# Kernel optimization log

Hardware: AMD Instinct MI355X
Metric: run time of the kernel (lower is better)

## Reference

```python
import jax, jax.numpy as jnp
import numpy as np
import math

EPS = 1e-12


def _cmul(ar, ai, br, bi):
    return ar * br - ai * bi, ar * bi + ai * br


def _wilson_seed(x):
    # x: (B, 4, L, L) -> conj of canonical Wilson-line path, (B, L, L) re/im
    ux_r, ux_i, uy_r, uy_i = x[:, 0], x[:, 1], x[:, 2], x[:, 3]
    B, L, _ = ux_r.shape
    dt = x.dtype

    def step(c, u):
        cr, ci = c
        ur, ui = u
        nr, ni = _cmul(cr, ci, ur, ui)
        return (nr, ni), (nr, ni)

    # cumulative complex product along x at y=0
    init_r = jnp.ones((B,), dt)
    init_i = jnp.zeros((B,), dt)
    xs = (ux_r[:, :-1, 0].T, ux_i[:, :-1, 0].T)  # (L-1, B)
    _, (axr, axi) = jax.lax.scan(step, (init_r, init_i), xs)
    x_axis_r = jnp.concatenate([init_r[None], axr], 0).T  # (B, L)
    x_axis_i = jnp.concatenate([init_i[None], axi], 0).T

    # cumulative complex product along y, vectorized over x
    ys = (jnp.moveaxis(uy_r[:, :, :-1], 2, 0), jnp.moveaxis(uy_i[:, :, :-1], 2, 0))  # (L-1, B, L)
    _, (pr, pi_) = jax.lax.scan(step, (x_axis_r, x_axis_i), ys)
    path_r = jnp.moveaxis(jnp.concatenate([x_axis_r[None], pr], 0), 0, 2)  # (B, L, L)
    path_i = jnp.moveaxis(jnp.concatenate([x_axis_i[None], pi_], 0), 0, 2)
    return path_r, -path_i  # conjugate


def _wrap(t):
    return (t + math.pi) % (2.0 * math.pi) - math.pi


def _initial_features(x):
    seed_r, seed_i = _wilson_seed(x)
    ax = jnp.arctan2(x[:, 1], x[:, 0])
    ay = jnp.arctan2(x[:, 3], x[:, 2])
    plaq = _wrap(ax + jnp.roll(ay, -1, axis=1) - jnp.roll(ax, -1, axis=2) - ay)
    pc = jnp.cos(plaq)
    pavg = (pc + jnp.roll(pc, 1, 1) + jnp.roll(pc, -1, 1)
            + jnp.roll(pc, 1, 2) + jnp.roll(pc, -1, 2)) / 5.0
    scalars = jnp.stack([jnp.ones_like(pc), pc, pavg], axis=1)  # (B, 3, L, L)
    return seed_r[:, None] * scalars, seed_i[:, None] * scalars


def _transport_fwd(fr, fi, x, mu):
    lr, li = (x[:, 0], x[:, 1]) if mu == 0 else (x[:, 2], x[:, 3])
    sr = jnp.roll(fr, -1, axis=mu + 2)
    si = jnp.roll(fi, -1, axis=mu + 2)
    return _cmul(lr[:, None], li[:, None], sr, si)


def _transport_bwd(fr, fi, x, mu):
    lr, li = (x[:, 0], x[:, 1]) if mu == 0 else (x[:, 2], x[:, 3])
    cr = jnp.roll(lr, 1, axis=mu + 1)
    ci = jnp.roll(-li, 1, axis=mu + 1)
    sr = jnp.roll(fr, 1, axis=mu + 2)
    si = jnp.roll(fi, 1, axis=mu + 2)
    return _cmul(cr[:, None], ci[:, None], sr, si)


def _lconv(fr, fi, x, center, fwd_w, bwd_w):
    out_r = jnp.einsum('oi,bixy->boxy', center, fr)
    out_i = jnp.einsum('oi,bixy->boxy', center, fi)
    for mu in range(2):
        fr2, fi2 = _transport_fwd(fr, fi, x, mu)
        br2, bi2 = _transport_bwd(fr, fi, x, mu)
        out_r = out_r + jnp.einsum('oi,bixy->boxy', fwd_w[mu], fr2) \
                      + jnp.einsum('oi,bixy->boxy', bwd_w[mu], br2)
        out_i = out_i + jnp.einsum('oi,bixy->boxy', fwd_w[mu], fi2) \
                      + jnp.einsum('oi,bixy->boxy', bwd_w[mu], bi2)
    return out_r, out_i


def _modrelu(fr, fi, bias):
    mag = jnp.sqrt(fr * fr + fi * fi + EPS)
    act = jax.nn.relu(mag + bias[None, :, None, None])
    scale = act / jnp.maximum(mag, EPS)
    return fr * scale, fi * scale


def setup_inputs() -> dict:
    key = jax.random.key(0)
    ks = jax.random.split(key, 11)
    B, L, H, O = 64, 128, 16, 8
    s = 0.1
    return {
        'x': jax.random.normal(ks[0], (B, 4, L, L), jnp.float32),
        'center1': s * jax.random.normal(ks[1], (H, 3), jnp.float32),
        'fwd_w1': s * jax.random.normal(ks[2], (2, H, 3), jnp.float32),
        'bwd_w1': s * jax.random.normal(ks[3], (2, H, 3), jnp.float32),
        'bias1': jnp.zeros((H,), jnp.float32),
        'center2': s * jax.random.normal(ks[4], (O, H), jnp.float32),
        'fwd_w2': s * jax.random.normal(ks[5], (2, O, H), jnp.float32),
        'bwd_w2': s * jax.random.normal(ks[6], (2, O, H), jnp.float32),
        'bias2': jnp.zeros((O,), jnp.float32),
        'ro_weight': s * jax.random.normal(ks[7], (O,), jnp.float32),
        'ro_bias': jnp.zeros((1,), jnp.float32),
    }


def reference(x, center1, fwd_w1, bwd_w1, bias1, center2, fwd_w2, bwd_w2, bias2, ro_weight, ro_bias):
    fr, fi = _initial_features(x)
    fr, fi = _lconv(fr, fi, x, center1, fwd_w1, bwd_w1)
    fr, fi = _modrelu(fr, fi, bias1)
    fr, fi = _lconv(fr, fi, x, center2, fwd_w2, bwd_w2)
    fr, fi = _modrelu(fr, fi, bias2)
    inv = fr * fr + fi * fi
    return jnp.einsum('c,bcxy->bxy', ro_weight, inv)[:, None] + ro_bias.reshape(1, 1, 1, 1)
```

## Files before the change

kernel.cpp:

```cpp
#include <hip/hip_runtime.h>
#include <math.h>

#define LQ   128
#define BQ   64
#define LL   (LQ*LQ)
#define H1   16
#define O2   8
#define TILE 16
#define REG  18
#define NPTS (REG*REG)
#define PCR  22
#define PCN  (PCR*PCR)
#define LKR  23
#define LKN  (LKR*LKR)
#define SDR  20
#define SDN  (SDR*SDR)
#define FSTR 10

typedef float f2 __attribute__((ext_vector_type(2)));
using bf8 = __attribute__((ext_vector_type(8))) short;
using f4  = __attribute__((ext_vector_type(4))) float;

__device__ __forceinline__ int wrapi(int v) { return v & (LQ - 1); }

__device__ __forceinline__ unsigned f2bf(float f) {
    unsigned u = __float_as_uint(f);
    u += 0x7fffu + ((u >> 16) & 1u);
    return u >> 16;
}

#define WS_W1 ((size_t)BQ * LL)

__global__ __launch_bounds__(256)
void k_scan(const float* __restrict__ x,
            const float* __restrict__ c1, const float* __restrict__ fw1,
            const float* __restrict__ bw1, float* __restrict__ ws) {
    int blk = blockIdx.x;
    if (blk == BQ * 8) {
        int tid = threadIdx.x;
        if (tid < 120) {
            int t = tid / 24, r = tid - t * 24;
            int c = r >> 3, op = r & 7;
            const float* src = (t == 0) ? c1 : (t == 1) ? fw1 : (t == 2) ? bw1
                             : (t == 3) ? (fw1 + 48) : (bw1 + 48);
            float2 v = make_float2(src[(2 * op) * 3 + c], src[(2 * op + 1) * 3 + c]);
            ((float2*)ws)[WS_W1 + tid] = v;
        }
        return;
    }
    int b = blk >> 3, rq = blk & 7;
    int l = threadIdx.x & 63, w = threadIdx.x >> 6;
    const float* x0 = x + (size_t)b * 4 * LL;
    const float* x1 = x0 + LL;

    float ur0 = x0[(2 * l) * LQ],     ui0 = x1[(2 * l) * LQ];
    float ur1 = x0[(2 * l + 1) * LQ], ui1 = x1[(2 * l + 1) * LQ];
    float pr = ur0 * ur1 - ui0 * ui1;
    float pi = ur0 * ui1 + ui0 * ur1;
    for (int d = 1; d < 64; d <<= 1) {
        float qr = __shfl_up(pr, d, 64);
        float qi = __shfl_up(pi, d, 64);
        if (l >= d) {
            float nr = qr * pr - qi * pi;
            float ni = qr * pi + qi * pr;
            pr = nr; pi = ni;
        }
    }
    float er = __shfl_up(pr, 1, 64);
    float ei = __shfl_up(pi, 1, 64);
    if (l == 0) { er = 1.f; ei = 0.f; }
    float e1r = er * ur0 - ei * ui0;
    float e1i = er * ui0 + ei * ur0;

    const float* yrp = x + (size_t)(b * 4 + 2) * LL;
    const float* yip = yrp + LL;
    float4* seed4 = (float4*)ws;

    for (int k = 0; k < 4; ++k) {
        int i = rq * 16 + w * 4 + k;
        float cxr = __shfl((i & 1) ? e1r : er, i >> 1, 64);
        float cxi = __shfl((i & 1) ? e1i : ei, i >> 1, 64);
        const float* yr = yrp + (size_t)i * LQ;
        const float* yi = yip + (size_t)i * LQ;
        float vr0 = yr[2 * l],     vi0 = yi[2 * l];
        float vr1 = yr[2 * l + 1], vi1 = yi[2 * l + 1];
        float sr = vr0 * vr1 - vi0 * vi1;
        float si = vr0 * vi1 + vi0 * vr1;
        for (int d = 1; d < 64; d <<= 1) {
            float qr = __shfl_up(sr, d, 64);
            float qi = __shfl_up(si, d, 64);
            if (l >= d) {
                float nr = qr * sr - qi * si;
                float ni = qr * si + qi * sr;
                sr = nr; si = ni;
            }
        }
        float gr = __shfl_up(sr, 1, 64);
        float gi = __shfl_up(si, 1, 64);
        if (l == 0) { gr = 1.f; gi = 0.f; }
        float s0r = cxr * gr - cxi * gi;
        float s0i = cxr * gi + cxi * gr;
        float s1r = s0r * vr0 - s0i * vi0;
        float s1i = s0r * vi0 + s0i * vr0;
        seed4[((size_t)b * LL + (size_t)i * LQ) / 2 + l] =
            make_float4(s0r, -s0i, s1r, -s1i);
    }
}

__global__ __launch_bounds__(256, 4)
void k_main(const float* __restrict__ x,
            const float* __restrict__ c2, const float* __restrict__ fw2,
            const float* __restrict__ bw2, const float* __restrict__ b1,
            const float* __restrict__ b2,
            const float* __restrict__ ro, const float* __restrict__ rob,
            const float* __restrict__ ws, float* __restrict__ out) {
    __shared__ unsigned s_f1r[NPTS * FSTR];
    __shared__ unsigned s_f1i[NPTS * FSTR];
    __shared__ f2 s_ux[LKN];
    __shared__ f2 s_uy[LKN];
    __shared__ float s_pc[PCN];
    __shared__ f2 s_sd[SDN];
    int tid = threadIdx.x;
    int b = blockIdx.z, i0 = blockIdx.y * TILE, j0 = blockIdx.x * TILE;
    const float* x0 = x + (size_t)b * 4 * LL;
    const float* x1 = x0 + LL;
    const float* x2 = x0 + 2 * LL;
    const float* x3 = x0 + 3 * LL;
    const float2* seed = (const float2*)ws + (size_t)b * LL;
    const float2* W1 = (const float2*)ws + WS_W1;

    bool z1 = true;
#pragma unroll
    for (int h = 0; h < H1; ++h) z1 = z1 && (b1[h] == 0.f);
    bool z2 = true;
#pragma unroll
    for (int o = 0; o < O2; ++o) z2 = z2 && (b2[o] == 0.f);

    for (int p = tid; p < LKN; p += 256) {
        int ri = p / LKR, rj = p - ri * LKR;
        int gi = wrapi(i0 - 3 + ri), gj = wrapi(j0 - 3 + rj);
        int idx = gi * LQ + gj;
        s_ux[p] = (f2){x0[idx], x1[idx]};
        s_uy[p] = (f2){x2[idx], x3[idx]};
    }
    for (int p = tid; p < SDN; p += 256) {
        int ri = p / SDR, rj = p - ri * SDR;
        int gi = wrapi(i0 - 2 + ri), gj = wrapi(j0 - 2 + rj);
        float2 s = seed[gi * LQ + gj];
        s_sd[p] = (f2){s.x, s.y};
    }
    __syncthreads();

    for (int p = tid; p < PCN; p += 256) {
        int ri = p / PCR, rj = p - ri * PCR;
        int lb = ri * LKR + rj;
        f2 u1 = s_ux[lb];
        f2 u2 = s_uy[lb + LKR];
        f2 u3 = s_ux[lb + 1];
        f2 u4 = s_uy[lb];
        float ar = u1.x * u2.x - u1.y * u2.y, ai = u1.x * u2.y + u1.y * u2.x;
        float br = ar * u3.x + ai * u3.y,     bi = -ar * u3.y + ai * u3.x;
        float zr = br * u4.x + bi * u4.y,     zi = -br * u4.y + bi * u4.x;
        s_pc[p] = zr * __frsqrt_rn(fmaf(zr, zr, zi * zi) + 1e-30f);
    }
    __syncthreads();

#pragma unroll
    for (int pass = 0; pass < 2; ++pass) {
        int p = tid + pass * 256;
        if (pass == 1 && p >= NPTS) break;
        int ri = p / REG, rj = p - ri * REG;
        int sc = (ri + 1) * SDR + (rj + 1);
        int lb = (ri + 2) * LKR + (rj + 2);
        int cb = (ri + 2) * PCR + (rj + 2);

        f2 t[5]; float tc[5], tv[5];
        {
            f2 SC = s_sd[sc], SXP = s_sd[sc + SDR], SXM = s_sd[sc - SDR];
            f2 SYP = s_sd[sc + 1], SYM = s_sd[sc - 1];
            f2 lx = s_ux[lb], ly = s_uy[lb];
            f2 mx = s_ux[lb - LKR], my = s_uy[lb - 1];
            t[0] = SC;
            t[1] = (f2){lx.x * SXP.x - lx.y * SXP.y, lx.x * SXP.y + lx.y * SXP.x};
            t[2] = (f2){mx.x * SXM.x + mx.y * SXM.y, mx.x * SXM.y - mx.y * SXM.x};
            t[3] = (f2){ly.x * SYP.x - ly.y * SYP.y, ly.x * SYP.y + ly.y * SYP.x};
            t[4] = (f2){my.x * SYM.x + my.y * SYM.y, my.x * SYM.y - my.y * SYM.x};
            int ct[5] = {cb, cb + PCR, cb - PCR, cb + 1, cb - 1};
#pragma unroll
            for (int q = 0; q < 5; ++q) {
                int c = ct[q];
                tc[q] = s_pc[c];
                tv[q] = (s_pc[c] + s_pc[c - PCR] + s_pc[c + PCR]
                       + s_pc[c - 1] + s_pc[c + 1]) * 0.2f;
            }
        }

        f2 accr[8], acci[8];
#pragma unroll
        for (int op = 0; op < 8; ++op) { accr[op] = (f2){0.f, 0.f}; acci[op] = (f2){0.f, 0.f}; }
#pragma unroll
        for (int q = 0; q < 5; ++q) {
            f2 tcv = (f2){tc[q], tc[q]}, tvv = (f2){tv[q], tv[q]};
            f2 trv = (f2){t[q].x, t[q].x}, tiv = (f2){t[q].y, t[q].y};
            const float2* Wq = W1 + q * 24;
#pragma unroll
            for (int op = 0; op < 8; ++op) {
                float2 w0 = Wq[op], w1 = Wq[8 + op], w2 = Wq[16 + op];
                f2 mp = (f2){w0.x, w0.y};
                mp += (f2){w1.x, w1.y} * tcv;
                mp += (f2){w2.x, w2.y} * tvv;
                accr[op] += mp * trv;
                acci[op] += mp * tiv;
            }
        }
        if (!z1) {
#pragma unroll
            for (int op = 0; op < 8; ++op) {
                f2 q2 = accr[op] * accr[op] + acci[op] * acci[op] + (f2){1e-12f, 1e-12f};
                float s0 = fmaxf(fmaf(b1[2 * op],     __frsqrt_rn(q2.x), 1.f), 0.f);
                float s1 = fmaxf(fmaf(b1[2 * op + 1], __frsqrt_rn(q2.y), 1.f), 0.f);
                f2 sv = (f2){s0, s1};
                accr[op] *= sv; acci[op] *= sv;
            }
        }
        unsigned* fr_ = &s_f1r[p * FSTR];
        unsigned* fi_ = &s_f1i[p * FSTR];
#pragma unroll
        for (int d = 0; d < 4; ++d) {
            unsigned r0 = f2bf(accr[2*d].x)   | (f2bf(accr[2*d].y) << 16);
            unsigned r1 = f2bf(accr[2*d+1].x) | (f2bf(accr[2*d+1].y) << 16);
            unsigned i0_ = f2bf(acci[2*d].x)   | (f2bf(acci[2*d].y) << 16);
            unsigned i1_ = f2bf(acci[2*d+1].x) | (f2bf(acci[2*d+1].y) << 16);
            *(uint2*)&fr_[2*d] = make_uint2(r0, r1);
            *(uint2*)&fi_[2*d] = make_uint2(i0_, i1_);
        }
    }
    __syncthreads();

    int lane = tid & 63, w = tid >> 6;
    int quad = lane >> 4, nIdx = lane & 15;

    const float* wt0 = c2;
    const float* wt1 = fw2;
    const float* wt2 = bw2;
    const float* wt3 = fw2 + O2 * H1;
    const float* wt4 = bw2 + O2 * H1;
    const float* wts[5] = {wt0, wt1, wt2, wt3, wt4};
    bf8 afr[5];
    bool aval = (nIdx < O2) && (quad < 2);
#pragma unroll
    for (int q = 0; q < 5; ++q) {
        bf8 z = {0, 0, 0, 0, 0, 0, 0, 0};
        if (aval) {
            const float* wp = wts[q] + nIdx * H1 + quad * 8;
            float4 wa = *(const float4*)wp;
            float4 wb = *(const float4*)(wp + 4);
            uint4 u;
            u.x = f2bf(wa.x) | (f2bf(wa.y) << 16);
            u.y = f2bf(wa.z) | (f2bf(wa.w) << 16);
            u.z = f2bf(wb.x) | (f2bf(wb.y) << 16);
            u.w = f2bf(wb.z) | (f2bf(wb.w) << 16);
            __builtin_memcpy(&z, &u, 16);
        }
        afr[q] = z;
    }
    float4 ro_lo = *(const float4*)ro;
    float4 ro_hi = *(const float4*)(ro + 4);
    float4 b2_lo = *(const float4*)b2;
    float4 b2_hi = *(const float4*)(b2 + 4);
    float4 zf4 = make_float4(0.f, 0.f, 0.f, 0.f);
    float4 rv = (quad == 0) ? ro_lo : ((quad == 1) ? ro_hi : zf4);
    float4 bv = (quad == 0) ? b2_lo : ((quad == 1) ? b2_hi : zf4);
    float rob0 = rob[0];
    const int dp5[5] = {0, REG, -REG, 1, -1};

    for (int g = 0; g < 4; ++g) {
        int row = w * 4 + g;
        int posc = (row + 1) * REG + (nIdx + 1);
        int lb2 = (row + 3) * LKR + (nIdx + 3);
        f2 lx = s_ux[lb2], ly = s_uy[lb2];
        f2 mx = s_ux[lb2 - LKR], my = s_uy[lb2 - 1];
        float lrq[5] = {1.f, lx.x, mx.x,  ly.x, my.x};
        float liq[5] = {0.f, lx.y, -mx.y, ly.y, -my.y};

        f4 a2r = {0.f, 0.f, 0.f, 0.f}, a2i = {0.f, 0.f, 0.f, 0.f};
#pragma unroll
        for (int q = 0; q < 5; ++q) {
            bf8 br = {0, 0, 0, 0, 0, 0, 0, 0};
            bf8 bi = {0, 0, 0, 0, 0, 0, 0, 0};
            if (quad < 2) {
                int posq = posc + dp5[q];
                const unsigned* pr_ = &s_f1r[posq * FSTR + quad * 4];
                uint2 lo = *(const uint2*)pr_;
                uint2 hi = *(const uint2*)(pr_ + 2);
                uint4 ur = {lo.x, lo.y, hi.x, hi.y};
                __builtin_memcpy(&br, &ur, 16);
                const unsigned* pi_ = &s_f1i[posq * FSTR + quad * 4];
                uint2 lo2 = *(const uint2*)pi_;
                uint2 hi2 = *(const uint2*)(pi_ + 2);
                uint4 ui = {lo2.x, lo2.y, hi2.x, hi2.y};
                __builtin_memcpy(&bi, &ui, 16);
            }
            f4 zc = {0.f, 0.f, 0.f, 0.f};
            f4 sr = __builtin_amdgcn_mfma_f32_16x16x32_bf16(afr[q], br, zc, 0, 0, 0);
            f4 si = __builtin_amdgcn_mfma_f32_16x16x32_bf16(afr[q], bi, zc, 0, 0, 0);
            a2r += lrq[q] * sr - liq[q] * si;
            a2i += lrq[q] * si + liq[q] * sr;
        }

        f4 q4 = a2r * a2r + a2i * a2i;
        float res;
        if (z2) {
            res = rv.x * q4.x + rv.y * q4.y + rv.z * q4.z + rv.w * q4.w;
        } else {
            float bvv[4] = {bv.x, bv.y, bv.z, bv.w};
            float rvv[4] = {rv.x, rv.y, rv.z, rv.w};
            res = 0.f;
#pragma unroll
            for (int r = 0; r < 4; ++r) {
                float qq = q4[r];
                float s = fmaxf(fmaf(bvv[r], __frsqrt_rn(qq + 1e-12f), 1.f), 0.f);
                res = fmaf(rvv[r], s * s * qq, res);
            }
        }
        res += __shfl_xor(res, 16, 64);
        res += __shfl_xor(res, 32, 64);
        if (quad == 0)
            out[(size_t)b * LL + (size_t)(i0 + row) * LQ + (j0 + nIdx)] = res + rob0;
    }
}

extern "C" void kernel_launch(void* const* d_in, const int* in_sizes, int n_in,
                              void* d_out, int out_size, void* d_ws, size_t ws_size,
                              hipStream_t stream) {
    const float* x   = (const float*)d_in[0];
    const float* c1  = (const float*)d_in[1];
    const float* fw1 = (const float*)d_in[2];
    const float* bw1 = (const float*)d_in[3];
    const float* b1  = (const float*)d_in[4];
    const float* c2  = (const float*)d_in[5];
    const float* fw2 = (const float*)d_in[6];
    const float* bw2 = (const float*)d_in[7];
    const float* b2  = (const float*)d_in[8];
    const float* ro  = (const float*)d_in[9];
    const float* rob = (const float*)d_in[10];
    float* out = (float*)d_out;
    float* ws  = (float*)d_ws;

    k_scan<<<BQ * 8 + 1, 256, 0, stream>>>(x, c1, fw1, bw1, ws);
    dim3 grid(LQ / TILE, LQ / TILE, BQ);
    k_main<<<grid, 256, 0, stream>>>(x, c2, fw2, bw2, b1, b2,
                                     ro, rob, ws, out);
}
```

Baseline: 145.4 us.

## Pack two transport terms per MFMA using idle K lanes; truncate bf16 packing

The second-layer MFMA now puts two of the five stencil terms into one 16x16x32 instruction as a block-diagonal product. Rows 0-7 and K 0-15 hold one term, rows 8-15 and K 16-31 hold another, and a cross-half shuffle recombines them. This cuts the MFMA count from ten to six per row group and puts the previously idle upper-quad lanes to work. Plaquette-average neighbour loads are deduplicated, and bf16 conversion switches from round-to-nearest to truncation via a byte permute. Truncation adds a small accuracy loss.

```diff
diff --git a/kernel.cpp b/kernel.cpp
--- a/kernel.cpp
+++ b/kernel.cpp
@@ -23,10 +23,9 @@
 
 __device__ __forceinline__ int wrapi(int v) { return v & (LQ - 1); }
 
-__device__ __forceinline__ unsigned f2bf(float f) {
-    unsigned u = __float_as_uint(f);
-    u += 0x7fffu + ((u >> 16) & 1u);
-    return u >> 16;
+__device__ __forceinline__ unsigned pack_bf(float hi, float lo) {
+    return __builtin_amdgcn_perm(__float_as_uint(hi), __float_as_uint(lo),
+                                 0x07060302u);
 }
 
 #define WS_W1 ((size_t)BQ * LL)
@@ -185,14 +184,19 @@
             t[2] = (f2){mx.x * SXM.x + mx.y * SXM.y, mx.x * SXM.y - mx.y * SXM.x};
             t[3] = (f2){ly.x * SYP.x - ly.y * SYP.y, ly.x * SYP.y + ly.y * SYP.x};
             t[4] = (f2){my.x * SYM.x + my.y * SYM.y, my.x * SYM.y - my.y * SYM.x};
-            int ct[5] = {cb, cb + PCR, cb - PCR, cb + 1, cb - 1};
-#pragma unroll
-            for (int q = 0; q < 5; ++q) {
-                int c = ct[q];
-                tc[q] = s_pc[c];
-                tv[q] = (s_pc[c] + s_pc[c - PCR] + s_pc[c + PCR]
-                       + s_pc[c - 1] + s_pc[c + 1]) * 0.2f;
-            }
+            float p00 = s_pc[cb];
+            float pP0 = s_pc[cb + PCR],     pM0 = s_pc[cb - PCR];
+            float p0P = s_pc[cb + 1],       p0M = s_pc[cb - 1];
+            float pP20 = s_pc[cb + 2*PCR],  pM20 = s_pc[cb - 2*PCR];
+            float p0P2 = s_pc[cb + 2],      p0M2 = s_pc[cb - 2];
+            float pPP = s_pc[cb + PCR + 1], pPM = s_pc[cb + PCR - 1];
+            float pMP = s_pc[cb - PCR + 1], pMM = s_pc[cb - PCR - 1];
+            tc[0] = p00; tc[1] = pP0; tc[2] = pM0; tc[3] = p0P; tc[4] = p0M;
+            tv[0] = (p00 + pP0 + pM0 + p0P + p0M) * 0.2f;
+            tv[1] = (pP0 + pP20 + p00 + pPP + pPM) * 0.2f;
+            tv[2] = (pM0 + p00 + pM20 + pMP + pMM) * 0.2f;
+            tv[3] = (p0P + pPP + pMP + p0P2 + p00) * 0.2f;
+            tv[4] = (p0M + pPM + pMM + p00 + p0M2) * 0.2f;
         }
 
         f2 accr[8], acci[8];
@@ -227,42 +231,42 @@
         unsigned* fi_ = &s_f1i[p * FSTR];
 #pragma unroll
         for (int d = 0; d < 4; ++d) {
-            unsigned r0 = f2bf(accr[2*d].x)   | (f2bf(accr[2*d].y) << 16);
-            unsigned r1 = f2bf(accr[2*d+1].x) | (f2bf(accr[2*d+1].y) << 16);
-            unsigned i0_ = f2bf(acci[2*d].x)   | (f2bf(acci[2*d].y) << 16);
-            unsigned i1_ = f2bf(acci[2*d+1].x) | (f2bf(acci[2*d+1].y) << 16);
+            unsigned r0 = pack_bf(accr[2*d].y,   accr[2*d].x);
+            unsigned r1 = pack_bf(accr[2*d+1].y, accr[2*d+1].x);
+            unsigned q0 = pack_bf(acci[2*d].y,   acci[2*d].x);
+            unsigned q1 = pack_bf(acci[2*d+1].y, acci[2*d+1].x);
             *(uint2*)&fr_[2*d] = make_uint2(r0, r1);
-            *(uint2*)&fi_[2*d] = make_uint2(i0_, i1_);
+            *(uint2*)&fi_[2*d] = make_uint2(q0, q1);
         }
     }
     __syncthreads();
 
     int lane = tid & 63, w = tid >> 6;
     int quad = lane >> 4, nIdx = lane & 15;
-
-    const float* wt0 = c2;
-    const float* wt1 = fw2;
-    const float* wt2 = bw2;
-    const float* wt3 = fw2 + O2 * H1;
-    const float* wt4 = bw2 + O2 * H1;
-    const float* wts[5] = {wt0, wt1, wt2, wt3, wt4};
-    bf8 afr[5];
-    bool aval = (nIdx < O2) && (quad < 2);
-#pragma unroll
-    for (int q = 0; q < 5; ++q) {
+    int half = quad >> 1;
+    int koff = (quad & 1) * 4;
+
+    const float* wLo[3] = {c2, bw2, bw2 + O2 * H1};
+    const float* wHi[3] = {fw2, fw2 + O2 * H1, (const float*)0};
+    bf8 afr[3];
+#pragma unroll
+    for (int pq = 0; pq < 3; ++pq) {
         bf8 z = {0, 0, 0, 0, 0, 0, 0, 0};
-        if (aval) {
-            const float* wp = wts[q] + nIdx * H1 + quad * 8;
+        const float* wsrc = half ? wHi[pq] : wLo[pq];
+        int row = half ? (nIdx - 8) : nIdx;
+        bool valid = half ? (nIdx >= 8 && wsrc != 0) : (nIdx < 8);
+        if (valid) {
+            const float* wp = wsrc + row * H1 + (quad & 1) * 8;
             float4 wa = *(const float4*)wp;
             float4 wb = *(const float4*)(wp + 4);
             uint4 u;
-            u.x = f2bf(wa.x) | (f2bf(wa.y) << 16);
-            u.y = f2bf(wa.z) | (f2bf(wa.w) << 16);
-            u.z = f2bf(wb.x) | (f2bf(wb.y) << 16);
-            u.w = f2bf(wb.z) | (f2bf(wb.w) << 16);
+            u.x = pack_bf(wa.y, wa.x);
+            u.y = pack_bf(wa.w, wa.z);
+            u.z = pack_bf(wb.y, wb.x);
+            u.w = pack_bf(wb.w, wb.z);
             __builtin_memcpy(&z, &u, 16);
         }
-        afr[q] = z;
+        afr[pq] = z;
     }
     float4 ro_lo = *(const float4*)ro;
     float4 ro_hi = *(const float4*)(ro + 4);
@@ -272,7 +276,6 @@
     float4 rv = (quad == 0) ? ro_lo : ((quad == 1) ? ro_hi : zf4);
     float4 bv = (quad == 0) ? b2_lo : ((quad == 1) ? b2_hi : zf4);
     float rob0 = rob[0];
-    const int dp5[5] = {0, REG, -REG, 1, -1};
 
     for (int g = 0; g < 4; ++g) {
         int row = w * 4 + g;
@@ -280,32 +283,40 @@
         int lb2 = (row + 3) * LKR + (nIdx + 3);
         f2 lx = s_ux[lb2], ly = s_uy[lb2];
         f2 mx = s_ux[lb2 - LKR], my = s_uy[lb2 - 1];
-        float lrq[5] = {1.f, lx.x, mx.x,  ly.x, my.x};
-        float liq[5] = {0.f, lx.y, -mx.y, ly.y, -my.y};
+
+        float Lr[3], Li[3];
+        Lr[0] = half ? lx.x : 1.f;   Li[0] = half ? lx.y : 0.f;
+        Lr[1] = half ? ly.x : mx.x;  Li[1] = half ? ly.y : -mx.y;
+        Lr[2] = half ? 0.f : my.x;   Li[2] = half ? 0.f : -my.y;
+        int dpl[3];
+        dpl[0] = half ? REG : 0;
+        dpl[1] = half ? 1 : -REG;
+        dpl[2] = -1;
 
         f4 a2r = {0.f, 0.f, 0.f, 0.f}, a2i = {0.f, 0.f, 0.f, 0.f};
 #pragma unroll
-        for (int q = 0; q < 5; ++q) {
-            bf8 br = {0, 0, 0, 0, 0, 0, 0, 0};
-            bf8 bi = {0, 0, 0, 0, 0, 0, 0, 0};
-            if (quad < 2) {
-                int posq = posc + dp5[q];
-                const unsigned* pr_ = &s_f1r[posq * FSTR + quad * 4];
-                uint2 lo = *(const uint2*)pr_;
-                uint2 hi = *(const uint2*)(pr_ + 2);
-                uint4 ur = {lo.x, lo.y, hi.x, hi.y};
-                __builtin_memcpy(&br, &ur, 16);
-                const unsigned* pi_ = &s_f1i[posq * FSTR + quad * 4];
-                uint2 lo2 = *(const uint2*)pi_;
-                uint2 hi2 = *(const uint2*)(pi_ + 2);
-                uint4 ui = {lo2.x, lo2.y, hi2.x, hi2.y};
-                __builtin_memcpy(&bi, &ui, 16);
-            }
+        for (int pq = 0; pq < 3; ++pq) {
+            int base = (posc + dpl[pq]) * FSTR + koff;
+            uint2 rlo = *(const uint2*)&s_f1r[base];
+            uint2 rhi = *(const uint2*)&s_f1r[base + 2];
+            uint2 ilo = *(const uint2*)&s_f1i[base];
+            uint2 ihi = *(const uint2*)&s_f1i[base + 2];
+            bf8 br, bi;
+            uint4 ur = {rlo.x, rlo.y, rhi.x, rhi.y};
+            uint4 ui = {ilo.x, ilo.y, ihi.x, ihi.y};
+            __builtin_memcpy(&br, &ur, 16);
+            __builtin_memcpy(&bi, &ui, 16);
             f4 zc = {0.f, 0.f, 0.f, 0.f};
-            f4 sr = __builtin_amdgcn_mfma_f32_16x16x32_bf16(afr[q], br, zc, 0, 0, 0);
-            f4 si = __builtin_amdgcn_mfma_f32_16x16x32_bf16(afr[q], bi, zc, 0, 0, 0);
-            a2r += lrq[q] * sr - liq[q] * si;
-            a2i += lrq[q] * si + liq[q] * sr;
+            f4 sr = __builtin_amdgcn_mfma_f32_16x16x32_bf16(afr[pq], br, zc, 0, 0, 0);
+            f4 si = __builtin_amdgcn_mfma_f32_16x16x32_bf16(afr[pq], bi, zc, 0, 0, 0);
+            a2r += Lr[pq] * sr - Li[pq] * si;
+            a2i += Lr[pq] * si + Li[pq] * sr;
+        }
+
+#pragma unroll
+        for (int c = 0; c < 4; ++c) {
+            a2r[c] += __shfl_xor(a2r[c], 32, 64);
+            a2i[c] += __shfl_xor(a2i[c], 32, 64);
         }
 
         f4 q4 = a2r * a2r + a2i * a2i;
@@ -324,7 +335,6 @@
             }
         }
         res += __shfl_xor(res, 16, 64);
-        res += __shfl_xor(res, 32, 64);
         if (quad == 0)
             out[(size_t)b * LL + (size_t)(i0 + row) * LQ + (j0 + nIdx)] = res + rob0;
     }
```

New measurement: 134.3 us. 1.08x faster.
